# Kernel optimization log

Hardware: AMD Instinct MI355X
Metric: run time of the kernel (lower is better)

## Reference

```python
import jax, jax.numpy as jnp
import numpy as np

B, S, A, H, E = 8192, 256, 64, 1024, 8
IN = S + A
OUT = S + 1


def setup_inputs() -> dict:
    key = jax.random.key(0)
    ks = jax.random.split(key, 8)
    state = jax.random.normal(ks[0], (B, S), dtype=jnp.float32)
    action = jax.random.normal(ks[1], (B, A), dtype=jnp.float32)
    idx = jax.random.randint(ks[2], (B,), 0, E, dtype=jnp.int32)
    # Kaiming-ish scaling to keep activations sane
    W1 = jax.random.normal(ks[3], (E, IN, H), dtype=jnp.float32) / np.sqrt(IN)
    b1 = jnp.zeros((E, H), dtype=jnp.float32)
    W2 = jax.random.normal(ks[4], (E, H, H), dtype=jnp.float32) / np.sqrt(H)
    b2 = jnp.zeros((E, H), dtype=jnp.float32)
    W3 = jax.random.normal(ks[5], (E, H, OUT), dtype=jnp.float32) / np.sqrt(H)
    b3 = jnp.zeros((E, OUT), dtype=jnp.float32)
    return {"state": state, "action": action, "idx": idx,
            "W1": W1, "b1": b1, "W2": W2, "b2": b2, "W3": W3, "b3": b3}


def reference(state, action, idx, W1, b1, W2, b2, W3, b3):
    # Dense-MoE style: run all E experts on the full batch, then select the
    # per-sample expert output chosen by idx (matches masked gather/scatter
    # in the torch predict loop).
    x = jnp.concatenate([state, action], axis=-1)                  # [B, IN]
    h = jax.nn.relu(jnp.einsum('bi,eih->beh', x, W1) + b1)         # [B, E, H]
    h = jax.nn.relu(jnp.einsum('beh,ehk->bek', h, W2) + b2)        # [B, E, H]
    out = jnp.einsum('beh,eho->beo', h, W3) + b3                   # [B, E, S+1]
    sel = jnp.take_along_axis(out, idx[:, None, None], axis=1)[:, 0]  # [B, S+1]
    s_dim = state.shape[-1]
    delta = sel[:, :s_dim]
    reward = sel[:, s_dim:]
    next_state = state + delta
    return next_state, reward
```

## Files before the change

### kernel.cpp

```cpp
#include <hip/hip_runtime.h>
#include <stdint.h>

#define B_SZ   8192
#define IN_DIM 320
#define H_DIM  1024
#define E_NUM  8
#define OUT_DIM 257
#define TM     64
#define MAXT   (B_SZ / TM + E_NUM)

typedef __bf16 bf16x8 __attribute__((ext_vector_type(8)));
typedef float  f32x4  __attribute__((ext_vector_type(4)));

typedef unsigned int __attribute__((address_space(1))) as1_uint;
typedef unsigned int __attribute__((address_space(3))) as3_uint;

__device__ __forceinline__ void gload_lds16(const void* g, void* l) {
    __builtin_amdgcn_global_load_lds((const as1_uint*)g, (as3_uint*)l, 16, 0, 0);
}

__device__ __forceinline__ unsigned short f2bf(float f) {
    unsigned int u = __float_as_uint(f);
    return (unsigned short)((u + 0x7fffu + ((u >> 16) & 1u)) >> 16);
}

__global__ __launch_bounds__(256)
void k_prep(const float* __restrict__ state, const float* __restrict__ action,
            const int* __restrict__ idx,
            const float* __restrict__ W1, const float* __restrict__ W2,
            const float* __restrict__ W3,
            unsigned short* __restrict__ xb, unsigned short* __restrict__ w1t,
            unsigned short* __restrict__ w2t, unsigned short* __restrict__ w3t,
            int* __restrict__ order, int* __restrict__ te,
            int* __restrict__ tp0, int* __restrict__ tcnt) {
    __shared__ float tile[64][65];
    __shared__ int scnt[16][E_NUM];
    int bid = blockIdx.x, tid = threadIdx.x;

    if (bid == 0) {
        int shard = tid & 15;
        if (tid < 128) ((int*)scnt)[tid] = 0;
        __syncthreads();
        for (int b = tid; b < B_SZ; b += 256) atomicAdd(&scnt[shard][idx[b]], 1);
        __syncthreads();
        if (tid == 0) {
            int pos = 0, tt = 0;
            for (int e = 0; e < E_NUM; e++) {
                int start = pos;
                for (int s = 0; s < 16; s++) { int c = scnt[s][e]; scnt[s][e] = pos; pos += c; }
                int tot = pos - start;
                for (int st = 0; st < tot; st += TM) {
                    te[tt] = e; tp0[tt] = start + st; tcnt[tt] = min(TM, tot - st); tt++;
                }
            }
            for (; tt < MAXT; tt++) { te[tt] = 0; tp0[tt] = 0; tcnt[tt] = 0; }
        }
        __syncthreads();
        for (int b = tid; b < B_SZ; b += 256) {
            int e = idx[b];
            int p = atomicAdd(&scnt[shard][e], 1);
            order[p] = b;
        }
        return;
    }

    if (bid <= 2560) {
        int q = (bid - 1) * 256 + tid;
        int b = q / 80, j = q % 80;
        float4 v = (j < 64) ? ((const float4*)state)[b * 64 + j]
                            : ((const float4*)action)[b * 16 + (j - 64)];
        ushort4 o;
        o.x = f2bf(v.x); o.y = f2bf(v.y); o.z = f2bf(v.z); o.w = f2bf(v.w);
        ((ushort4*)xb)[q] = o;
        return;
    }

    if (bid < 5761) {
        int e, kt, nt, K, Nsrc, dstRows;
        const float* src; unsigned short* dst;
        if (bid < 3201) {
            int r = bid - 2561; e = r / 80; int m = r % 80; kt = m / 16; nt = m % 16;
            K = IN_DIM; Nsrc = H_DIM; dstRows = H_DIM; src = W1; dst = w1t;
        } else if (bid < 5249) {
            int r = bid - 3201; e = r / 256; int m = r % 256; kt = m / 16; nt = m % 16;
            K = H_DIM; Nsrc = H_DIM; dstRows = H_DIM; src = W2; dst = w2t;
        } else {
            int r = bid - 5249; e = r / 64; int m = r % 64; kt = m / 4; nt = m % 4;
            K = H_DIM; Nsrc = OUT_DIM; dstRows = 320; src = W3; dst = w3t;
        }
        int k0 = kt * 64, n0 = nt * 64;
        const float* s = src + (size_t)e * K * Nsrc;
        unsigned short* d = dst + (size_t)e * dstRows * K;
        int tx = tid & 63, ty = tid >> 6;
        for (int rr = ty; rr < 64; rr += 4)
            tile[rr][tx] = s[(size_t)(k0 + rr) * Nsrc + (n0 + tx)];
        __syncthreads();
        for (int rr = ty; rr < 64; rr += 4)
            d[(size_t)(n0 + rr) * K + (k0 + tx)] = f2bf(tile[tx][rr]);
        return;
    }

    int i = (bid - 5761) * 256 + tid;
    int e = i >> 10, k = i & 1023;
    w3t[((size_t)e * 320 + 256) * H_DIM + k] =
        f2bf(W3[((size_t)e * H_DIM + k) * OUT_DIM + 256]);
}

template <int K, int TN, int WN, bool GATHER, int MODE>
__global__ __launch_bounds__(256, 2)
void k_gemm(const unsigned short* __restrict__ Abase,
            const unsigned short* __restrict__ Wt, int wtRows,
            const float* __restrict__ bias, int bstride,
            unsigned short* __restrict__ Hout,
            float* __restrict__ Out, const float* __restrict__ state,
            const int* __restrict__ order,
            const int* __restrict__ te, const int* __restrict__ tp0,
            const int* __restrict__ tcnt) {
    constexpr int NI  = K / 32;
    constexpr int NF  = WN / 16;
    constexpr int ABY = 64 * 64;
    constexpr int BBY = TN * 64;
    constexpr int STG = ABY + BBY;
    __shared__ __align__(16) char lds[2 * STG];

    int t = blockIdx.x;
    int cnt = tcnt[t];
    if (cnt == 0) return;
    int e = te[t], p0 = tp0[t];
    int n0 = blockIdx.y * TN;
    int tid = threadIdx.x;
    int w = tid >> 6, lane = tid & 63;

    int r  = tid >> 2;
    int cg = (tid & 3) ^ ((r >> 1) & 3);
    int rc = r < cnt ? r : cnt - 1;
    long arow = GATHER ? order[p0 + rc] : (p0 + rc);
    const unsigned short* aP = Abase + (size_t)arow * K + cg * 8;
    const unsigned short* bP = Wt + ((size_t)e * wtRows + n0 + r) * K + cg * 8;

    auto stage = [&](int k0, int sb) {
        gload_lds16(aP + k0, lds + sb + tid * 16);
        gload_lds16(bP + k0, lds + sb + ABY + tid * 16);
        if (TN == 128)
            gload_lds16(bP + (size_t)64 * K + k0, lds + sb + ABY + 4096 + tid * 16);
    };

    f32x4 acc[4][NF];
#pragma unroll
    for (int i = 0; i < 4; i++)
#pragma unroll
        for (int j = 0; j < NF; j++) acc[i][j] = (f32x4)0.f;

    const int fm   = lane & 15;
    const int kc   = lane >> 4;
    const int koff = ((kc ^ ((fm >> 1) & 3)) * 8);

    stage(0, 0);
    for (int it = 0; it < NI; ++it) {
        __syncthreads();
        if (it + 1 < NI) stage((it + 1) * 32, ((it + 1) & 1) * STG);
        const unsigned short* As = (const unsigned short*)(lds + (it & 1) * STG);
        const unsigned short* Bs = As + ABY / 2;

        bf16x8 af[4], bf[NF];
#pragma unroll
        for (int i = 0; i < 4; i++)
            af[i] = *(const bf16x8*)&As[(i * 16 + fm) * 32 + koff];
#pragma unroll
        for (int j = 0; j < NF; j++)
            bf[j] = *(const bf16x8*)&Bs[(w * WN + j * 16 + fm) * 32 + koff];
#pragma unroll
        for (int i = 0; i < 4; i++)
#pragma unroll
            for (int j = 0; j < NF; j++)
                acc[i][j] = __builtin_amdgcn_mfma_f32_16x16x32_bf16(
                    af[i], bf[j], acc[i][j], 0, 0, 0);
    }

    int col = lane & 15, rq = lane >> 4;
#pragma unroll
    for (int j = 0; j < NF; j++) {
        int n = n0 + w * WN + j * 16 + col;
        float bv = (MODE == 0) ? bias[e * bstride + n]
                               : ((n <= 256) ? bias[e * bstride + n] : 0.f);
#pragma unroll
        for (int i = 0; i < 4; i++) {
#pragma unroll
            for (int rr = 0; rr < 4; rr++) {
                int m = i * 16 + rq * 4 + rr;
                if (m < cnt) {
                    float v = acc[i][j][rr] + bv;
                    if (MODE == 0) {
                        Hout[(size_t)(p0 + m) * H_DIM + n] = f2bf(fmaxf(v, 0.f));
                    } else {
                        int row = order[p0 + m];
                        if (n < 256) {
                            size_t o = (size_t)row * 256 + n;
                            Out[o] = state[o] + v;
                        } else if (n == 256) {
                            Out[(size_t)B_SZ * 256 + row] = v;
                        }
                    }
                }
            }
        }
    }
}

extern "C" void kernel_launch(void* const* d_in, const int* in_sizes, int n_in,
                              void* d_out, int out_size, void* d_ws, size_t ws_size,
                              hipStream_t stream) {
    const float* state  = (const float*)d_in[0];
    const float* action = (const float*)d_in[1];
    const int*   idx    = (const int*)d_in[2];
    const float* W1     = (const float*)d_in[3];
    const float* b1     = (const float*)d_in[4];
    const float* W2     = (const float*)d_in[5];
    const float* b2     = (const float*)d_in[6];
    const float* W3     = (const float*)d_in[7];
    const float* b3     = (const float*)d_in[8];
    float* out = (float*)d_out;

    char* ws = (char*)d_ws;
    size_t off = 0;
    auto alloc = [&](size_t bytes) -> void* {
        void* p = ws + off;
        off = (off + bytes + 255) & ~(size_t)255;
        return p;
    };
    unsigned short* xb  = (unsigned short*)alloc((size_t)B_SZ * IN_DIM * 2);
    unsigned short* w1t = (unsigned short*)alloc((size_t)E_NUM * H_DIM * IN_DIM * 2);
    unsigned short* w2t = (unsigned short*)alloc((size_t)E_NUM * H_DIM * H_DIM * 2);
    unsigned short* w3t = (unsigned short*)alloc((size_t)E_NUM * 320 * H_DIM * 2);
    unsigned short* h1  = (unsigned short*)alloc((size_t)B_SZ * H_DIM * 2);
    unsigned short* h2  = (unsigned short*)alloc((size_t)B_SZ * H_DIM * 2);
    int* order = (int*)alloc(B_SZ * 4);
    int* te    = (int*)alloc(MAXT * 4);
    int* tp0   = (int*)alloc(MAXT * 4);
    int* tcnt  = (int*)alloc(MAXT * 4);

    k_prep<<<5793, 256, 0, stream>>>(state, action, idx, W1, W2, W3,
                                     xb, w1t, w2t, w3t, order, te, tp0, tcnt);

    k_gemm<IN_DIM, 128, 32, true, 0><<<dim3(MAXT, 8), 256, 0, stream>>>(
        xb, w1t, H_DIM, b1, H_DIM, h1, nullptr, nullptr, order, te, tp0, tcnt);
    k_gemm<H_DIM, 128, 32, false, 0><<<dim3(MAXT, 8), 256, 0, stream>>>(
        h1, w2t, H_DIM, b2, H_DIM, h2, nullptr, nullptr, order, te, tp0, tcnt);
    k_gemm<H_DIM, 64, 16, false, 1><<<dim3(MAXT, 5), 256, 0, stream>>>(
        h2, w3t, 320, b3, OUT_DIM, nullptr, out, state, order, te, tp0, tcnt);
}
```

Baseline: 225.0 us.

## Enlarge GEMM block tile to 128x128 with 2x2 warp grid

```diff
diff --git a/kernel.cpp b/kernel.cpp
--- a/kernel.cpp
+++ b/kernel.cpp
@@ -6,8 +6,9 @@
 #define H_DIM  1024
 #define E_NUM  8
 #define OUT_DIM 257
-#define TM     64
+#define TM     128
 #define MAXT   (B_SZ / TM + E_NUM)
+#define W3ROWS 384
 
 typedef __bf16 bf16x8 __attribute__((ext_vector_type(8)));
 typedef float  f32x4  __attribute__((ext_vector_type(4)));
@@ -86,7 +87,7 @@
             K = H_DIM; Nsrc = H_DIM; dstRows = H_DIM; src = W2; dst = w2t;
         } else {
             int r = bid - 5249; e = r / 64; int m = r % 64; kt = m / 4; nt = m % 4;
-            K = H_DIM; Nsrc = OUT_DIM; dstRows = 320; src = W3; dst = w3t;
+            K = H_DIM; Nsrc = OUT_DIM; dstRows = W3ROWS; src = W3; dst = w3t;
         }
         int k0 = kt * 64, n0 = nt * 64;
         const float* s = src + (size_t)e * K * Nsrc;
@@ -102,11 +103,11 @@
 
     int i = (bid - 5761) * 256 + tid;
     int e = i >> 10, k = i & 1023;
-    w3t[((size_t)e * 320 + 256) * H_DIM + k] =
+    w3t[((size_t)e * W3ROWS + 256) * H_DIM + k] =
         f2bf(W3[((size_t)e * H_DIM + k) * OUT_DIM + 256]);
 }
 
-template <int K, int TN, int WN, bool GATHER, int MODE>
+template <int K, bool GATHER, int MODE>
 __global__ __launch_bounds__(256, 2)
 void k_gemm(const unsigned short* __restrict__ Abase,
             const unsigned short* __restrict__ Wt, int wtRows,
@@ -117,43 +118,46 @@
             const int* __restrict__ te, const int* __restrict__ tp0,
             const int* __restrict__ tcnt) {
     constexpr int NI  = K / 32;
-    constexpr int NF  = WN / 16;
-    constexpr int ABY = 64 * 64;
-    constexpr int BBY = TN * 64;
-    constexpr int STG = ABY + BBY;
+    constexpr int ABY = 128 * 64;
+    constexpr int STG = 2 * ABY;
     __shared__ __align__(16) char lds[2 * STG];
 
     int t = blockIdx.x;
     int cnt = tcnt[t];
     if (cnt == 0) return;
     int e = te[t], p0 = tp0[t];
-    int n0 = blockIdx.y * TN;
+    int n0 = blockIdx.y * 128;
     int tid = threadIdx.x;
     int w = tid >> 6, lane = tid & 63;
 
     int r  = tid >> 2;
     int cg = (tid & 3) ^ ((r >> 1) & 3);
-    int rc = r < cnt ? r : cnt - 1;
-    long arow = GATHER ? order[p0 + rc] : (p0 + rc);
-    const unsigned short* aP = Abase + (size_t)arow * K + cg * 8;
-    const unsigned short* bP = Wt + ((size_t)e * wtRows + n0 + r) * K + cg * 8;
+    int rc0 = r < cnt ? r : cnt - 1;
+    int rc1 = (r + 64) < cnt ? (r + 64) : cnt - 1;
+    long ar0 = GATHER ? order[p0 + rc0] : (p0 + rc0);
+    long ar1 = GATHER ? order[p0 + rc1] : (p0 + rc1);
+    const unsigned short* aP0 = Abase + (size_t)ar0 * K + cg * 8;
+    const unsigned short* aP1 = Abase + (size_t)ar1 * K + cg * 8;
+    const unsigned short* bP0 = Wt + ((size_t)e * wtRows + n0 + r) * K + cg * 8;
+    const unsigned short* bP1 = bP0 + (size_t)64 * K;
 
     auto stage = [&](int k0, int sb) {
-        gload_lds16(aP + k0, lds + sb + tid * 16);
-        gload_lds16(bP + k0, lds + sb + ABY + tid * 16);
-        if (TN == 128)
-            gload_lds16(bP + (size_t)64 * K + k0, lds + sb + ABY + 4096 + tid * 16);
+        gload_lds16(aP0 + k0, lds + sb + tid * 16);
+        gload_lds16(aP1 + k0, lds + sb + 4096 + tid * 16);
+        gload_lds16(bP0 + k0, lds + sb + ABY + tid * 16);
+        gload_lds16(bP1 + k0, lds + sb + ABY + 4096 + tid * 16);
     };
 
-    f32x4 acc[4][NF];
+    f32x4 acc[4][4];
 #pragma unroll
     for (int i = 0; i < 4; i++)
 #pragma unroll
-        for (int j = 0; j < NF; j++) acc[i][j] = (f32x4)0.f;
-
+        for (int j = 0; j < 4; j++) acc[i][j] = (f32x4)0.f;
+
+    const int m_off = (w >> 1) * 64, n_off = (w & 1) * 64;
     const int fm   = lane & 15;
     const int kc   = lane >> 4;
-    const int koff = ((kc ^ ((fm >> 1) & 3)) * 8);
+    const int koff = (kc ^ ((fm >> 1) & 3)) * 8;
 
     stage(0, 0);
     for (int it = 0; it < NI; ++it) {
@@ -162,32 +166,32 @@
         const unsigned short* As = (const unsigned short*)(lds + (it & 1) * STG);
         const unsigned short* Bs = As + ABY / 2;
 
-        bf16x8 af[4], bf[NF];
+        bf16x8 af[4], bf[4];
 #pragma unroll
         for (int i = 0; i < 4; i++)
-            af[i] = *(const bf16x8*)&As[(i * 16 + fm) * 32 + koff];
-#pragma unroll
-        for (int j = 0; j < NF; j++)
-            bf[j] = *(const bf16x8*)&Bs[(w * WN + j * 16 + fm) * 32 + koff];
+            af[i] = *(const bf16x8*)&As[(m_off + i * 16 + fm) * 32 + koff];
+#pragma unroll
+        for (int j = 0; j < 4; j++)
+            bf[j] = *(const bf16x8*)&Bs[(n_off + j * 16 + fm) * 32 + koff];
 #pragma unroll
         for (int i = 0; i < 4; i++)
 #pragma unroll
-            for (int j = 0; j < NF; j++)
+            for (int j = 0; j < 4; j++)
                 acc[i][j] = __builtin_amdgcn_mfma_f32_16x16x32_bf16(
                     af[i], bf[j], acc[i][j], 0, 0, 0);
     }
 
     int col = lane & 15, rq = lane >> 4;
 #pragma unroll
-    for (int j = 0; j < NF; j++) {
-        int n = n0 + w * WN + j * 16 + col;
+    for (int j = 0; j < 4; j++) {
+        int n = n0 + n_off + j * 16 + col;
         float bv = (MODE == 0) ? bias[e * bstride + n]
                                : ((n <= 256) ? bias[e * bstride + n] : 0.f);
 #pragma unroll
         for (int i = 0; i < 4; i++) {
 #pragma unroll
             for (int rr = 0; rr < 4; rr++) {
-                int m = i * 16 + rq * 4 + rr;
+                int m = m_off + i * 16 + rq * 4 + rr;
                 if (m < cnt) {
                     float v = acc[i][j][rr] + bv;
                     if (MODE == 0) {
@@ -231,7 +235,7 @@
     unsigned short* xb  = (unsigned short*)alloc((size_t)B_SZ * IN_DIM * 2);
     unsigned short* w1t = (unsigned short*)alloc((size_t)E_NUM * H_DIM * IN_DIM * 2);
     unsigned short* w2t = (unsigned short*)alloc((size_t)E_NUM * H_DIM * H_DIM * 2);
-    unsigned short* w3t = (unsigned short*)alloc((size_t)E_NUM * 320 * H_DIM * 2);
+    unsigned short* w3t = (unsigned short*)alloc((size_t)E_NUM * W3ROWS * H_DIM * 2);
     unsigned short* h1  = (unsigned short*)alloc((size_t)B_SZ * H_DIM * 2);
     unsigned short* h2  = (unsigned short*)alloc((size_t)B_SZ * H_DIM * 2);
     int* order = (int*)alloc(B_SZ * 4);
@@ -242,10 +246,10 @@
     k_prep<<<5793, 256, 0, stream>>>(state, action, idx, W1, W2, W3,
                                      xb, w1t, w2t, w3t, order, te, tp0, tcnt);
 
-    k_gemm<IN_DIM, 128, 32, true, 0><<<dim3(MAXT, 8), 256, 0, stream>>>(
+    k_gemm<IN_DIM, true, 0><<<dim3(MAXT, 8), 256, 0, stream>>>(
         xb, w1t, H_DIM, b1, H_DIM, h1, nullptr, nullptr, order, te, tp0, tcnt);
-    k_gemm<H_DIM, 128, 32, false, 0><<<dim3(MAXT, 8), 256, 0, stream>>>(
+    k_gemm<H_DIM, false, 0><<<dim3(MAXT, 8), 256, 0, stream>>>(
         h1, w2t, H_DIM, b2, H_DIM, h2, nullptr, nullptr, order, te, tp0, tcnt);
-    k_gemm<H_DIM, 64, 16, false, 1><<<dim3(MAXT, 5), 256, 0, stream>>>(
-        h2, w3t, 320, b3, OUT_DIM, nullptr, out, state, order, te, tp0, tcnt);
-}
+    k_gemm<H_DIM, false, 1><<<dim3(MAXT, 3), 256, 0, stream>>>(
+        h2, w3t, W3ROWS, b3, OUT_DIM, nullptr, out, state, order, te, tp0, tcnt);
+}
```

Result: slower. 236.8 us (+5.2%).
